# Kernel tuning notes

Hardware: AMD Instinct MI355X
Metric: run time of the kernel (lower is better)

## Reference

```python
import jax, jax.numpy as jnp
import numpy as np

B, T, C, NH = 4, 2048, 1024, 16
D = C // NH  # 64


def setup_inputs() -> dict:
    key = jax.random.key(0)
    ks = jax.random.split(key, 6)
    x = jax.random.normal(ks[0], (B, T, C), dtype=jnp.float32)
    # realistic RoPE tables: interleaved cos/sin over T positions, D head dim
    inv_freq = 1.0 / (10000.0 ** (np.arange(0, D, 2, dtype=np.float32) / D))
    ang = np.arange(T, dtype=np.float32)[:, None] * inv_freq[None, :]  # (T, D/2)
    ang = np.repeat(ang, 2, axis=-1)  # (T, D) interleaved
    pe_cos = jnp.asarray(np.cos(ang))[None, None]  # (1,1,T,D)
    pe_sin = jnp.asarray(np.sin(ang))[None, None]
    pe_scale = jax.random.uniform(ks[1], (1, 1, T, D), dtype=jnp.float32, minval=0.5, maxval=1.5)
    mask = 0.1 * jax.random.normal(ks[2], (1, B, T, T), dtype=jnp.float32)
    w_qkv = jax.random.normal(ks[3], (3 * C, C), dtype=jnp.float32) * (C ** -0.5)
    b_qkv = jax.random.normal(ks[4], (3 * C,), dtype=jnp.float32) * 0.02
    return {"x": x, "pe_cos": pe_cos, "pe_sin": pe_sin, "pe_scale": pe_scale,
            "mask": mask, "w_qkv": w_qkv, "b_qkv": b_qkv}


def _rotate_interleaved(u):
    # even positions <- -odd, odd positions <- even (RoPE interleave)
    u2 = u.reshape(u.shape[:-1] + (-1, 2))
    rot = jnp.stack([-u2[..., 1], u2[..., 0]], axis=-1)
    return rot.reshape(u.shape)


def reference(x, pe_cos, pe_sin, pe_scale, mask, w_qkv, b_qkv):
    b, t, c = x.shape
    qkv = x @ w_qkv.T + b_qkv  # (b, t, 3c)
    q, k, v = jnp.split(qkv, 3, axis=-1)
    # (b, t, nh, d) -> (b, nh, t, d)
    to_heads = lambda u: u.reshape(b, t, NH, D).transpose(0, 2, 1, 3)
    q, k, v = to_heads(q), to_heads(k), to_heads(v)
    # pe tensors (1,1,t,d) broadcast over (b,nh,t,d)
    q = (q * pe_cos + _rotate_interleaved(q) * pe_sin) * pe_scale
    k = (k * pe_cos + _rotate_interleaved(k) * pe_sin) / pe_scale
    scale = 1.0 / ((2.0 * D) ** 0.5)  # original uses scale=1/sqrt(2d)
    scores = jnp.einsum('bhqd,bhkd->bhqk', q, k) * scale
    # torch layout was (nh, b, t, t) + mask (1, b, t, t): mask broadcasts over heads
    scores = scores + jnp.swapaxes(mask, 0, 1)  # mask -> (b, 1, t, t)
    attn = jax.nn.softmax(scores, axis=-1)
    out = jnp.einsum('bhqk,bhkd->bhqd', attn, v)  # (b, nh, t, d)
    return out.transpose(0, 2, 1, 3).reshape(b, t, c)
```

## Files before the change

### kernel.cpp

```cpp
#include <hip/hip_runtime.h>
#include <math.h>

#define NB 4
#define NT 2048
#define NC 1024
#define NHEADS 16
#define HDIM 64

typedef __attribute__((ext_vector_type(8))) _Float16 half8v;
typedef __attribute__((ext_vector_type(2))) __fp16 fp16x2;
typedef __attribute__((ext_vector_type(4))) float f32x4;

#define LOG2E 1.4426950408889634f

__device__ inline unsigned short f2h(float f) {
    _Float16 h = (_Float16)f;
    return __builtin_bit_cast(unsigned short, h);
}
__device__ inline float h2f(unsigned short u) {
    return (float)__builtin_bit_cast(_Float16, u);
}
__device__ inline float exp2fast(float x) {
#if __has_builtin(__builtin_amdgcn_exp2f)
    return __builtin_amdgcn_exp2f(x);
#else
    return exp2f(x);
#endif
}
__device__ inline unsigned int pack2h(float a, float b) {
    fp16x2 p = __builtin_amdgcn_cvt_pkrtz(a, b);
    return __builtin_bit_cast(unsigned int, p);
}

#define AS1C(p) ((const __attribute__((address_space(1))) unsigned int*)(unsigned long long)(const void*)(p))
#define AS3P(p) ((__attribute__((address_space(3))) unsigned int*)(unsigned int)(unsigned long long)(void*)(p))
#define GLL16(gp, lp) __builtin_amdgcn_global_load_lds(AS1C(gp), AS3P(lp), 16, 0, 0)

__global__ __launch_bounds__(256) void conv_f16_kernel(
    const float* __restrict__ in, unsigned short* __restrict__ out, int n4)
{
    const int i = blockIdx.x * 256 + threadIdx.x;
    if (i >= n4) return;
    const float4 f = ((const float4*)in)[i];
    ushort4 h;
    h.x = f2h(f.x); h.y = f2h(f.y); h.z = f2h(f.z); h.w = f2h(f.w);
    ((ushort4*)out)[i] = h;
}

__global__ __launch_bounds__(256) void mask_conv_kernel(
    const float* __restrict__ in, unsigned short* __restrict__ out)
{
    const size_t i = (size_t)blockIdx.x * 256 + threadIdx.x;
    const int row = (int)(i >> 9);
    const int c4 = (int)(i & 511);
    const int ktb = c4 >> 4;
    const int fr = c4 & 15;
    const float* ip = in + (size_t)row * NT + ktb * 64 + fr;
    ushort4 o;
    o.x = f2h(ip[0] * LOG2E);
    o.y = f2h(ip[16] * LOG2E);
    o.z = f2h(ip[32] * LOG2E);
    o.w = f2h(ip[48] * LOG2E);
    ((ushort4*)out)[i] = o;
}

__global__ __launch_bounds__(256) void qkv_gemm_kernel(
    const unsigned short* __restrict__ xf, const unsigned short* __restrict__ wf,
    const float* __restrict__ bias, const float* __restrict__ pe_cos,
    const float* __restrict__ pe_sin, const float* __restrict__ pe_scale,
    unsigned short* __restrict__ qb, unsigned short* __restrict__ kb,
    unsigned short* __restrict__ vtb)
{
    __shared__ __align__(16) unsigned short Ah[128 * 32];
    __shared__ __align__(16) unsigned short Bh[128 * 32];

    const int tid = threadIdx.x;
    const int w = tid >> 6, lane = tid & 63;
    const int g = lane >> 4, fr = lane & 15;
    const int wr = w >> 1, wc = w & 1;

    const int bid = blockIdx.x;
    const int s = (bid & 7) * 192 + (bid >> 3);
    const int m0 = (s & 63) * 128, n0 = (s >> 6) * 128;

    const int c0 = tid, c1 = tid + 256;
    const int r0 = c0 >> 2, r1 = c1 >> 2;
    const int cb0 = ((c0 & 3) * 16) ^ (((r0 >> 1) & 3) << 4);
    const int cb1 = ((c1 & 3) * 16) ^ (((r1 >> 1) & 3) << 4);
    const unsigned short* px0 = xf + (size_t)(m0 + r0) * NC + (cb0 >> 1);
    const unsigned short* px1 = xf + (size_t)(m0 + r1) * NC + (cb1 >> 1);
    const unsigned short* pw0 = wf + (size_t)(n0 + r0) * NC + (cb0 >> 1);
    const unsigned short* pw1 = wf + (size_t)(n0 + r1) * NC + (cb1 >> 1);

    f32x4 acc[4][4];
#pragma unroll
    for (int m = 0; m < 4; ++m)
#pragma unroll
        for (int n = 0; n < 4; ++n) acc[m][n] = (f32x4){0.f, 0.f, 0.f, 0.f};

    for (int k0 = 0; k0 < NC; k0 += 32) {
        __syncthreads();
        GLL16(px0 + k0, (char*)Ah + c0 * 16);
        GLL16(px1 + k0, (char*)Ah + c1 * 16);
        GLL16(pw0 + k0, (char*)Bh + c0 * 16);
        GLL16(pw1 + k0, (char*)Bh + c1 * 16);
        __syncthreads();

        half8v a_f[4], b_f[4];
#pragma unroll
        for (int m = 0; m < 4; ++m) {
            const int r = wr * 64 + m * 16 + fr;
            const int off = r * 64 + ((g * 16) ^ (((r >> 1) & 3) << 4));
            a_f[m] = *(const half8v*)((const char*)Ah + off);
        }
#pragma unroll
        for (int n = 0; n < 4; ++n) {
            const int r = wc * 64 + n * 16 + fr;
            const int off = r * 64 + ((g * 16) ^ (((r >> 1) & 3) << 4));
            b_f[n] = *(const half8v*)((const char*)Bh + off);
        }
#pragma unroll
        for (int m = 0; m < 4; ++m)
#pragma unroll
            for (int n = 0; n < 4; ++n)
                acc[m][n] = __builtin_amdgcn_mfma_f32_16x16x32_f16(a_f[m], b_f[n], acc[m][n], 0, 0, 0);
    }

    const float QSCL = 0.08838834764831845f * LOG2E;
#pragma unroll
    for (int n = 0; n < 4; ++n) {
        const int col = n0 + wc * 64 + n * 16 + fr;
        const int part = col >> 10;
        const int hh = (col & 1023) >> 6;
        const int dd = col & 63;
        const float bv = bias[col];
        if (part < 2) {
            unsigned short* outp = (part == 0) ? qb : kb;
#pragma unroll
            for (int m = 0; m < 4; ++m) {
                const int row0 = m0 + wr * 64 + m * 16 + 4 * g;
                const int bb = row0 >> 11;
                const int t0 = row0 & 2047;
#pragma unroll
                for (int j = 0; j < 4; ++j) {
                    const int t = t0 + j;
                    float val = acc[m][n][j] + bv;
                    const float partner = __shfl_xor(val, 1, 64);
                    const int pidx = t * HDIM + dd;
                    const float cc = pe_cos[pidx], ss = pe_sin[pidx], sc = pe_scale[pidx];
                    const float r = (dd & 1) ? (val * cc + partner * ss)
                                             : (val * cc - partner * ss);
                    val = (part == 0) ? (r * sc * QSCL) : (r / sc);
                    outp[(((size_t)bb * NHEADS + hh) * NT + t) * HDIM + dd] = f2h(val);
                }
            }
        } else {
            const int rowb = m0 + wr * 64;
            const int bb = rowb >> 11;
            const int tb = rowb & 2047;
            unsigned short* vp2 =
                &vtb[(((size_t)bb * NHEADS + hh) * HDIM + dd) * NT + tb];
#pragma unroll
            for (int j = 0; j < 4; ++j) {
                ushort4 sv;
                sv.x = f2h(acc[0][n][j] + bv);
                sv.y = f2h(acc[1][n][j] + bv);
                sv.z = f2h(acc[2][n][j] + bv);
                sv.w = f2h(acc[3][n][j] + bv);
                *(ushort4*)&vp2[(4 * g + j) * 4] = sv;
            }
        }
    }
}

__global__ __launch_bounds__(256) void attn_mfma_kernel(
    const unsigned short* __restrict__ qb, const unsigned short* __restrict__ kb,
    const unsigned short* __restrict__ vtb, const unsigned short* __restrict__ m16,
    float* __restrict__ out)
{
    __shared__ __align__(16) unsigned short Ks[2][64 * 64];
    __shared__ __align__(16) unsigned short Vs[2][64 * 64];
    __shared__ __align__(16) unsigned short Ps[4][16 * 64];

    const int tid = threadIdx.x;
    const int w = tid >> 6, lane = tid & 63;
    const int g = lane >> 4, fr = lane & 15;

    const int bid = blockIdx.x;
    const int s = (bid & 7) * 128 + (bid >> 3);
    const int q0 = (s & 15) * 128;
    const int h = (s >> 4) & 15;
    const int b = s >> 8;

    const size_t bh = (size_t)b * NHEADS + h;
    const unsigned short* qp = qb + (bh * NT + q0 + w * 32) * HDIM;
    const unsigned short* kp = kb + bh * NT * HDIM;
    const unsigned short* vtp = vtb + bh * HDIM * NT;
    const unsigned short* mp = m16 + ((size_t)b * NT + q0 + w * 32) * NT;

    const int sc0 = tid, sc1 = tid + 256;
    const int sr0 = sc0 >> 3, scb0 = ((sc0 & 7) * 16) ^ ((sr0 & 7) << 4);
    const int sr1 = sc1 >> 3, scb1 = ((sc1 & 7) * 16) ^ ((sr1 & 7) << 4);

#define STAGE(buf, kt)                                                          \
    do {                                                                        \
        const unsigned short* ktp_ = kp + (kt) * 64 * HDIM;                     \
        GLL16(ktp_ + sr0 * HDIM + (scb0 >> 1), (char*)Ks[buf] + sc0 * 16);      \
        GLL16(vtp + (size_t)sr0 * NT + (kt) * 64 + (scb0 >> 1),                 \
              (char*)Vs[buf] + sc0 * 16);                                       \
        GLL16(ktp_ + sr1 * HDIM + (scb1 >> 1), (char*)Ks[buf] + sc1 * 16);      \
        GLL16(vtp + (size_t)sr1 * NT + (kt) * 64 + (scb1 >> 1),                 \
              (char*)Vs[buf] + sc1 * 16);                                       \
    } while (0)

    half8v qf[2][2];
#pragma unroll
    for (int m = 0; m < 2; ++m)
#pragma unroll
        for (int kk = 0; kk < 2; ++kk)
            qf[m][kk] = *(const half8v*)(qp + (m * 16 + fr) * HDIM + kk * 32 + g * 8);

    f32x4 acc[2][4];
    float li[2][4], mi[2][4];
#pragma unroll
    for (int m = 0; m < 2; ++m)
#pragma unroll
        for (int j = 0; j < 4; ++j) {
            li[m][j] = 0.f; mi[m][j] = -3.0e38f;
            acc[m][j] = (f32x4){0.f, 0.f, 0.f, 0.f};
        }
    const float THR = 11.541560327111708f;

    STAGE(0, 0);
    __syncthreads();
    int cur = 0;

    for (int kt = 0; kt < NT / 64; ++kt) {
        if (kt + 1 < NT / 64) STAGE(cur ^ 1, kt + 1);

        half8v kf[4][2], vf[4][2];
#pragma unroll
        for (int nt = 0; nt < 4; ++nt) {
            const int r = nt * 16 + fr;
#pragma unroll
            for (int kk = 0; kk < 2; ++kk) {
                const int off = r * 128 + ((kk * 64 + g * 16) ^ ((r & 7) << 4));
                kf[nt][kk] = *(const half8v*)((const char*)Ks[cur] + off);
                vf[nt][kk] = *(const half8v*)((const char*)Vs[cur] + off);
            }
        }

#pragma unroll
        for (int m = 0; m < 2; ++m) {
            f32x4 Sm[4];
#pragma unroll
            for (int nt = 0; nt < 4; ++nt) {
                Sm[nt] = (f32x4){0.f, 0.f, 0.f, 0.f};
#pragma unroll
                for (int kk = 0; kk < 2; ++kk)
                    Sm[nt] = __builtin_amdgcn_mfma_f32_16x16x32_f16(qf[m][kk], kf[nt][kk], Sm[nt], 0, 0, 0);
            }

            float sv[4][4], rmj[4];
#pragma unroll
            for (int j = 0; j < 4; ++j) {
                const ushort4 mv = *(const ushort4*)(
                    mp + (size_t)(m * 16 + 4 * g + j) * NT + kt * 64 + fr * 4);
                sv[j][0] = Sm[0][j] + h2f(mv.x);
                sv[j][1] = Sm[1][j] + h2f(mv.y);
                sv[j][2] = Sm[2][j] + h2f(mv.z);
                sv[j][3] = Sm[3][j] + h2f(mv.w);
                rmj[j] = fmaxf(fmaxf(sv[j][0], sv[j][1]), fmaxf(sv[j][2], sv[j][3]));
            }

            const float worst = fmaxf(fmaxf(rmj[0] - mi[m][0], rmj[1] - mi[m][1]),
                                      fmaxf(rmj[2] - mi[m][2], rmj[3] - mi[m][3]));
            if (!__all(worst <= THR)) {
#pragma unroll
                for (int j = 0; j < 4; ++j) {
                    float rm = rmj[j];
                    rm = fmaxf(rm, __shfl_xor(rm, 1, 64));
                    rm = fmaxf(rm, __shfl_xor(rm, 2, 64));
                    rm = fmaxf(rm, __shfl_xor(rm, 4, 64));
                    rm = fmaxf(rm, __shfl_xor(rm, 8, 64));
                    const float mnew = fmaxf(mi[m][j], rm);
                    const float alpha = exp2fast(mi[m][j] - mnew);
                    li[m][j] *= alpha;
#pragma unroll
                    for (int dt = 0; dt < 4; ++dt) acc[m][dt][j] *= alpha;
                    mi[m][j] = mnew;
                }
            }

#pragma unroll
            for (int j = 0; j < 4; ++j) {
                const int prow = 4 * g + j;
                const float p0 = exp2fast(sv[j][0] - mi[m][j]);
                const float p1 = exp2fast(sv[j][1] - mi[m][j]);
                const float p2 = exp2fast(sv[j][2] - mi[m][j]);
                const float p3 = exp2fast(sv[j][3] - mi[m][j]);
                li[m][j] += (p0 + p1) + (p2 + p3);
                uint2 pw2;
                pw2.x = pack2h(p0, p1);
                pw2.y = pack2h(p2, p3);
                const int off = prow * 128 + ((fr * 8) ^ ((prow & 7) << 4));
                *(uint2*)((char*)Ps[w] + off) = pw2;
            }

            half8v pf[2];
#pragma unroll
            for (int kk = 0; kk < 2; ++kk) {
                const int off = fr * 128 + ((kk * 64 + g * 16) ^ ((fr & 7) << 4));
                pf[kk] = *(const half8v*)((const char*)Ps[w] + off);
            }
#pragma unroll
            for (int dt = 0; dt < 4; ++dt)
#pragma unroll
                for (int kk = 0; kk < 2; ++kk)
                    acc[m][dt] = __builtin_amdgcn_mfma_f32_16x16x32_f16(pf[kk], vf[dt][kk], acc[m][dt], 0, 0, 0);
        }

        __syncthreads();
        cur ^= 1;
    }

#pragma unroll
    for (int m = 0; m < 2; ++m)
#pragma unroll
        for (int j = 0; j < 4; ++j) {
            float lt = li[m][j];
            lt += __shfl_xor(lt, 1, 64);
            lt += __shfl_xor(lt, 2, 64);
            lt += __shfl_xor(lt, 4, 64);
            lt += __shfl_xor(lt, 8, 64);
            const float inv = 1.f / lt;
            const int t = q0 + w * 32 + m * 16 + 4 * g + j;
            float* op = out + (((size_t)b * NT + t) * NHEADS + h) * HDIM;
#pragma unroll
            for (int dt = 0; dt < 4; ++dt) op[dt * 16 + fr] = acc[m][dt][j] * inv;
        }
}

extern "C" void kernel_launch(void* const* d_in, const int* in_sizes, int n_in,
                              void* d_out, int out_size, void* d_ws, size_t ws_size,
                              hipStream_t stream) {
    const float* x        = (const float*)d_in[0];
    const float* pe_cos   = (const float*)d_in[1];
    const float* pe_sin   = (const float*)d_in[2];
    const float* pe_scale = (const float*)d_in[3];
    const float* mask     = (const float*)d_in[4];
    const float* w_qkv    = (const float*)d_in[5];
    const float* b_qkv    = (const float*)d_in[6];
    float* out = (float*)d_out;

    unsigned short* ws = (unsigned short*)d_ws;
    const size_t PER = (size_t)NB * NHEADS * NT * HDIM;
    unsigned short* qbuf = ws;
    unsigned short* kbuf = ws + PER;
    unsigned short* vtbuf = ws + 2 * PER;
    unsigned short* xbuf = ws + 3 * PER;
    unsigned short* wbuf = xbuf + (size_t)NB * NT * NC;
    unsigned short* maskbuf = ws + 3 * PER;

    conv_f16_kernel<<<8192, 256, 0, stream>>>(x, xbuf, (NB * NT * NC) / 4);
    conv_f16_kernel<<<3072, 256, 0, stream>>>(w_qkv, wbuf, (3 * NC * NC) / 4);
    qkv_gemm_kernel<<<1536, 256, 0, stream>>>(xbuf, wbuf, b_qkv,
                                              pe_cos, pe_sin, pe_scale,
                                              qbuf, kbuf, vtbuf);
    mask_conv_kernel<<<16384, 256, 0, stream>>>(mask, maskbuf);
    attn_mfma_kernel<<<1024, 256, 0, stream>>>(qbuf, kbuf, vtbuf, maskbuf, out);
}
```

Measured before the change: 262.5 us.

## Double per-block query tile and share one softmax max per wave tile

Each block now processes 256 query rows (64 per wave) instead of 128, halving the grid to 512 blocks so each staged K/V tile is reused by twice as many queries. The online-softmax running max is also changed from per-row to a single max shared across each 16-row wave tile, computed with a full-wave reduction. This cuts the per-row max reductions and rescaling work. The costs are a doubled accumulator register footprint, which may lower occupancy, and fewer blocks than may be needed to fill all CUs. Using a coarser shared max is still mathematically valid but can reduce numerical headroom when row maxima differ widely.

```diff
diff --git a/kernel.cpp b/kernel.cpp
--- a/kernel.cpp
+++ b/kernel.cpp
@@ -187,16 +187,16 @@
     const int g = lane >> 4, fr = lane & 15;
 
     const int bid = blockIdx.x;
-    const int s = (bid & 7) * 128 + (bid >> 3);
-    const int q0 = (s & 15) * 128;
-    const int h = (s >> 4) & 15;
-    const int b = s >> 8;
+    const int s = (bid & 7) * 64 + (bid >> 3);
+    const int q0 = (s & 7) * 256;
+    const int h = (s >> 3) & 15;
+    const int b = s >> 7;
 
     const size_t bh = (size_t)b * NHEADS + h;
-    const unsigned short* qp = qb + (bh * NT + q0 + w * 32) * HDIM;
+    const unsigned short* qp = qb + (bh * NT + q0 + w * 64) * HDIM;
     const unsigned short* kp = kb + bh * NT * HDIM;
     const unsigned short* vtp = vtb + bh * HDIM * NT;
-    const unsigned short* mp = m16 + ((size_t)b * NT + q0 + w * 32) * NT;
+    const unsigned short* mp = m16 + ((size_t)b * NT + q0 + w * 64) * NT;
 
     const int sc0 = tid, sc1 = tid + 256;
     const int sr0 = sc0 >> 3, scb0 = ((sc0 & 7) * 16) ^ ((sr0 & 7) << 4);
@@ -213,22 +213,24 @@
               (char*)Vs[buf] + sc1 * 16);                                       \
     } while (0)
 
-    half8v qf[2][2];
-#pragma unroll
-    for (int m = 0; m < 2; ++m)
+    half8v qf[4][2];
+#pragma unroll
+    for (int m = 0; m < 4; ++m)
 #pragma unroll
         for (int kk = 0; kk < 2; ++kk)
             qf[m][kk] = *(const half8v*)(qp + (m * 16 + fr) * HDIM + kk * 32 + g * 8);
 
-    f32x4 acc[2][4];
-    float li[2][4], mi[2][4];
-#pragma unroll
-    for (int m = 0; m < 2; ++m)
+    f32x4 acc[4][4];
+    float li[4][4], mi[4];
+#pragma unroll
+    for (int m = 0; m < 4; ++m) {
+        mi[m] = -3.0e38f;
 #pragma unroll
         for (int j = 0; j < 4; ++j) {
-            li[m][j] = 0.f; mi[m][j] = -3.0e38f;
+            li[m][j] = 0.f;
             acc[m][j] = (f32x4){0.f, 0.f, 0.f, 0.f};
         }
+    }
     const float THR = 11.541560327111708f;
 
     STAGE(0, 0);
@@ -251,7 +253,7 @@
         }
 
 #pragma unroll
-        for (int m = 0; m < 2; ++m) {
+        for (int m = 0; m < 4; ++m) {
             f32x4 Sm[4];
 #pragma unroll
             for (int nt = 0; nt < 4; ++nt) {
@@ -261,7 +263,8 @@
                     Sm[nt] = __builtin_amdgcn_mfma_f32_16x16x32_f16(qf[m][kk], kf[nt][kk], Sm[nt], 0, 0, 0);
             }
 
-            float sv[4][4], rmj[4];
+            float sv[4][4];
+            float smax = -3.4e38f;
 #pragma unroll
             for (int j = 0; j < 4; ++j) {
                 const ushort4 mv = *(const ushort4*)(
@@ -270,35 +273,37 @@
                 sv[j][1] = Sm[1][j] + h2f(mv.y);
                 sv[j][2] = Sm[2][j] + h2f(mv.z);
                 sv[j][3] = Sm[3][j] + h2f(mv.w);
-                rmj[j] = fmaxf(fmaxf(sv[j][0], sv[j][1]), fmaxf(sv[j][2], sv[j][3]));
-            }
-
-            const float worst = fmaxf(fmaxf(rmj[0] - mi[m][0], rmj[1] - mi[m][1]),
-                                      fmaxf(rmj[2] - mi[m][2], rmj[3] - mi[m][3]));
-            if (!__all(worst <= THR)) {
+                smax = fmaxf(smax,
+                             fmaxf(fmaxf(sv[j][0], sv[j][1]),
+                                   fmaxf(sv[j][2], sv[j][3])));
+            }
+
+            if (!__all(smax - mi[m] <= THR)) {
+                float rm = smax;
+                rm = fmaxf(rm, __shfl_xor(rm, 1, 64));
+                rm = fmaxf(rm, __shfl_xor(rm, 2, 64));
+                rm = fmaxf(rm, __shfl_xor(rm, 4, 64));
+                rm = fmaxf(rm, __shfl_xor(rm, 8, 64));
+                rm = fmaxf(rm, __shfl_xor(rm, 16, 64));
+                rm = fmaxf(rm, __shfl_xor(rm, 32, 64));
+                const float mnew = fmaxf(mi[m], rm);
+                const float alpha = exp2fast(mi[m] - mnew);
 #pragma unroll
                 for (int j = 0; j < 4; ++j) {
-                    float rm = rmj[j];
-                    rm = fmaxf(rm, __shfl_xor(rm, 1, 64));
-                    rm = fmaxf(rm, __shfl_xor(rm, 2, 64));
-                    rm = fmaxf(rm, __shfl_xor(rm, 4, 64));
-                    rm = fmaxf(rm, __shfl_xor(rm, 8, 64));
-                    const float mnew = fmaxf(mi[m][j], rm);
-                    const float alpha = exp2fast(mi[m][j] - mnew);
                     li[m][j] *= alpha;
 #pragma unroll
                     for (int dt = 0; dt < 4; ++dt) acc[m][dt][j] *= alpha;
-                    mi[m][j] = mnew;
                 }
+                mi[m] = mnew;
             }
 
 #pragma unroll
             for (int j = 0; j < 4; ++j) {
                 const int prow = 4 * g + j;
-                const float p0 = exp2fast(sv[j][0] - mi[m][j]);
-                const float p1 = exp2fast(sv[j][1] - mi[m][j]);
-                const float p2 = exp2fast(sv[j][2] - mi[m][j]);
-                const float p3 = exp2fast(sv[j][3] - mi[m][j]);
+                const float p0 = exp2fast(sv[j][0] - mi[m]);
+                const float p1 = exp2fast(sv[j][1] - mi[m]);
+                const float p2 = exp2fast(sv[j][2] - mi[m]);
+                const float p3 = exp2fast(sv[j][3] - mi[m]);
                 li[m][j] += (p0 + p1) + (p2 + p3);
                 uint2 pw2;
                 pw2.x = pack2h(p0, p1);
@@ -325,7 +330,7 @@
     }
 
 #pragma unroll
-    for (int m = 0; m < 2; ++m)
+    for (int m = 0; m < 4; ++m)
 #pragma unroll
         for (int j = 0; j < 4; ++j) {
             float lt = li[m][j];
@@ -334,7 +339,7 @@
             lt += __shfl_xor(lt, 4, 64);
             lt += __shfl_xor(lt, 8, 64);
             const float inv = 1.f / lt;
-            const int t = q0 + w * 32 + m * 16 + 4 * g + j;
+            const int t = q0 + w * 64 + m * 16 + 4 * g + j;
             float* op = out + (((size_t)b * NT + t) * NHEADS + h) * HDIM;
 #pragma unroll
             for (int dt = 0; dt < 4; ++dt) op[dt * 16 + fr] = acc[m][dt][j] * inv;
@@ -368,5 +373,5 @@
                                               pe_cos, pe_sin, pe_scale,
                                               qbuf, kbuf, vtbuf);
     mask_conv_kernel<<<16384, 256, 0, stream>>>(mask, maskbuf);
-    attn_mfma_kernel<<<1024, 256, 0, stream>>>(qbuf, kbuf, vtbuf, maskbuf, out);
-}
+    attn_mfma_kernel<<<512, 256, 0, stream>>>(qbuf, kbuf, vtbuf, maskbuf, out);
+}
```

Measured after the change: 346.9 us. 1.32x slower.

## Compute transposed scores in attention to keep P in registers, drop LDS round-trip

Applied to the files above, without the earlier changes.

The QK^T MFMA now runs with operands swapped, so each lane holds scores for one query row across several keys. P can then be packed straight into the A-operand of the PV MFMA instead of being written to and read back from LDS. The V^T store order and the mask layout are permuted to match, and the mask conversion uses the generic scaled conversion kernel with a plain row-major layout. Online softmax keeps one max/sum per lane with a wider shuffle reduction, which removes the LDS traffic and per-row bookkeeping but adds a cross-lane shuffle at the end.

```diff
diff --git a/kernel.cpp b/kernel.cpp
--- a/kernel.cpp
+++ b/kernel.cpp
@@ -10,6 +10,7 @@
 typedef __attribute__((ext_vector_type(8))) _Float16 half8v;
 typedef __attribute__((ext_vector_type(2))) __fp16 fp16x2;
 typedef __attribute__((ext_vector_type(4))) float f32x4;
+typedef __attribute__((ext_vector_type(4))) unsigned int u32x4;
 
 #define LOG2E 1.4426950408889634f
 
@@ -37,31 +38,16 @@
 #define GLL16(gp, lp) __builtin_amdgcn_global_load_lds(AS1C(gp), AS3P(lp), 16, 0, 0)
 
 __global__ __launch_bounds__(256) void conv_f16_kernel(
-    const float* __restrict__ in, unsigned short* __restrict__ out, int n4)
+    const float* __restrict__ in, unsigned short* __restrict__ out, int n4,
+    float scale)
 {
     const int i = blockIdx.x * 256 + threadIdx.x;
     if (i >= n4) return;
     const float4 f = ((const float4*)in)[i];
     ushort4 h;
-    h.x = f2h(f.x); h.y = f2h(f.y); h.z = f2h(f.z); h.w = f2h(f.w);
+    h.x = f2h(f.x * scale); h.y = f2h(f.y * scale);
+    h.z = f2h(f.z * scale); h.w = f2h(f.w * scale);
     ((ushort4*)out)[i] = h;
-}
-
-__global__ __launch_bounds__(256) void mask_conv_kernel(
-    const float* __restrict__ in, unsigned short* __restrict__ out)
-{
-    const size_t i = (size_t)blockIdx.x * 256 + threadIdx.x;
-    const int row = (int)(i >> 9);
-    const int c4 = (int)(i & 511);
-    const int ktb = c4 >> 4;
-    const int fr = c4 & 15;
-    const float* ip = in + (size_t)row * NT + ktb * 64 + fr;
-    ushort4 o;
-    o.x = f2h(ip[0] * LOG2E);
-    o.y = f2h(ip[16] * LOG2E);
-    o.z = f2h(ip[32] * LOG2E);
-    o.w = f2h(ip[48] * LOG2E);
-    ((ushort4*)out)[i] = o;
 }
 
 __global__ __launch_bounds__(256) void qkv_gemm_kernel(
@@ -160,15 +146,19 @@
             const int tb = rowb & 2047;
             unsigned short* vp2 =
                 &vtb[(((size_t)bb * NHEADS + hh) * HDIM + dd) * NT + tb];
-#pragma unroll
-            for (int j = 0; j < 4; ++j) {
-                ushort4 sv;
-                sv.x = f2h(acc[0][n][j] + bv);
-                sv.y = f2h(acc[1][n][j] + bv);
-                sv.z = f2h(acc[2][n][j] + bv);
-                sv.w = f2h(acc[3][n][j] + bv);
-                *(ushort4*)&vp2[(4 * g + j) * 4] = sv;
-            }
+            ushort4 s0a, s0b, s1a, s1b;
+            s0a.x = f2h(acc[0][n][0] + bv); s0a.y = f2h(acc[0][n][1] + bv);
+            s0a.z = f2h(acc[0][n][2] + bv); s0a.w = f2h(acc[0][n][3] + bv);
+            s0b.x = f2h(acc[2][n][0] + bv); s0b.y = f2h(acc[2][n][1] + bv);
+            s0b.z = f2h(acc[2][n][2] + bv); s0b.w = f2h(acc[2][n][3] + bv);
+            s1a.x = f2h(acc[1][n][0] + bv); s1a.y = f2h(acc[1][n][1] + bv);
+            s1a.z = f2h(acc[1][n][2] + bv); s1a.w = f2h(acc[1][n][3] + bv);
+            s1b.x = f2h(acc[3][n][0] + bv); s1b.y = f2h(acc[3][n][1] + bv);
+            s1b.z = f2h(acc[3][n][2] + bv); s1b.w = f2h(acc[3][n][3] + bv);
+            *(ushort4*)&vp2[8 * g]          = s0a;
+            *(ushort4*)&vp2[8 * g + 4]      = s0b;
+            *(ushort4*)&vp2[32 + 8 * g]     = s1a;
+            *(ushort4*)&vp2[32 + 8 * g + 4] = s1b;
         }
     }
 }
@@ -180,7 +170,6 @@
 {
     __shared__ __align__(16) unsigned short Ks[2][64 * 64];
     __shared__ __align__(16) unsigned short Vs[2][64 * 64];
-    __shared__ __align__(16) unsigned short Ps[4][16 * 64];
 
     const int tid = threadIdx.x;
     const int w = tid >> 6, lane = tid & 63;
@@ -196,7 +185,7 @@
     const unsigned short* qp = qb + (bh * NT + q0 + w * 32) * HDIM;
     const unsigned short* kp = kb + bh * NT * HDIM;
     const unsigned short* vtp = vtb + bh * HDIM * NT;
-    const unsigned short* mp = m16 + ((size_t)b * NT + q0 + w * 32) * NT;
+    const unsigned short* mp = m16 + ((size_t)b * NT + q0 + w * 32 + fr) * NT;
 
     const int sc0 = tid, sc1 = tid + 256;
     const int sr0 = sc0 >> 3, scb0 = ((sc0 & 7) * 16) ^ ((sr0 & 7) << 4);
@@ -221,14 +210,13 @@
             qf[m][kk] = *(const half8v*)(qp + (m * 16 + fr) * HDIM + kk * 32 + g * 8);
 
     f32x4 acc[2][4];
-    float li[2][4], mi[2][4];
-#pragma unroll
-    for (int m = 0; m < 2; ++m)
-#pragma unroll
-        for (int j = 0; j < 4; ++j) {
-            li[m][j] = 0.f; mi[m][j] = -3.0e38f;
-            acc[m][j] = (f32x4){0.f, 0.f, 0.f, 0.f};
-        }
+    float li[2], mi[2];
+#pragma unroll
+    for (int m = 0; m < 2; ++m) {
+        li[m] = 0.f; mi[m] = -3.0e38f;
+#pragma unroll
+        for (int dt = 0; dt < 4; ++dt) acc[m][dt] = (f32x4){0.f, 0.f, 0.f, 0.f};
+    }
     const float THR = 11.541560327111708f;
 
     STAGE(0, 0);
@@ -258,66 +246,63 @@
                 Sm[nt] = (f32x4){0.f, 0.f, 0.f, 0.f};
 #pragma unroll
                 for (int kk = 0; kk < 2; ++kk)
-                    Sm[nt] = __builtin_amdgcn_mfma_f32_16x16x32_f16(qf[m][kk], kf[nt][kk], Sm[nt], 0, 0, 0);
-            }
-
-            float sv[4][4], rmj[4];
-#pragma unroll
-            for (int j = 0; j < 4; ++j) {
-                const ushort4 mv = *(const ushort4*)(
-                    mp + (size_t)(m * 16 + 4 * g + j) * NT + kt * 64 + fr * 4);
-                sv[j][0] = Sm[0][j] + h2f(mv.x);
-                sv[j][1] = Sm[1][j] + h2f(mv.y);
-                sv[j][2] = Sm[2][j] + h2f(mv.z);
-                sv[j][3] = Sm[3][j] + h2f(mv.w);
-                rmj[j] = fmaxf(fmaxf(sv[j][0], sv[j][1]), fmaxf(sv[j][2], sv[j][3]));
-            }
-
-            const float worst = fmaxf(fmaxf(rmj[0] - mi[m][0], rmj[1] - mi[m][1]),
-                                      fmaxf(rmj[2] - mi[m][2], rmj[3] - mi[m][3]));
-            if (!__all(worst <= THR)) {
+                    Sm[nt] = __builtin_amdgcn_mfma_f32_16x16x32_f16(kf[nt][kk], qf[m][kk], Sm[nt], 0, 0, 0);
+            }
+
+            float sv[4][4];
+            float smax = -3.4e38f;
+            const unsigned short* mq = mp + (size_t)m * 16 * NT + kt * 64;
+#pragma unroll
+            for (int nt = 0; nt < 4; ++nt) {
+                const ushort4 mv = *(const ushort4*)(mq + nt * 16 + 4 * g);
+                sv[nt][0] = Sm[nt][0] + h2f(mv.x);
+                sv[nt][1] = Sm[nt][1] + h2f(mv.y);
+                sv[nt][2] = Sm[nt][2] + h2f(mv.z);
+                sv[nt][3] = Sm[nt][3] + h2f(mv.w);
+                smax = fmaxf(smax,
+                             fmaxf(fmaxf(sv[nt][0], sv[nt][1]),
+                                   fmaxf(sv[nt][2], sv[nt][3])));
+            }
+
+            if (!__all(smax - mi[m] <= THR)) {
+                float rm = smax;
+                rm = fmaxf(rm, __shfl_xor(rm, 1, 64));
+                rm = fmaxf(rm, __shfl_xor(rm, 2, 64));
+                rm = fmaxf(rm, __shfl_xor(rm, 4, 64));
+                rm = fmaxf(rm, __shfl_xor(rm, 8, 64));
+                rm = fmaxf(rm, __shfl_xor(rm, 16, 64));
+                rm = fmaxf(rm, __shfl_xor(rm, 32, 64));
+                const float mnew = fmaxf(mi[m], rm);
+                const float alpha = exp2fast(mi[m] - mnew);
+                li[m] *= alpha;
+#pragma unroll
+                for (int dt = 0; dt < 4; ++dt) acc[m][dt] *= alpha;
+                mi[m] = mnew;
+            }
+
+            float p[4][4];
+            float ps = 0.f;
+#pragma unroll
+            for (int nt = 0; nt < 4; ++nt)
 #pragma unroll
                 for (int j = 0; j < 4; ++j) {
-                    float rm = rmj[j];
-                    rm = fmaxf(rm, __shfl_xor(rm, 1, 64));
-                    rm = fmaxf(rm, __shfl_xor(rm, 2, 64));
-                    rm = fmaxf(rm, __shfl_xor(rm, 4, 64));
-                    rm = fmaxf(rm, __shfl_xor(rm, 8, 64));
-                    const float mnew = fmaxf(mi[m][j], rm);
-                    const float alpha = exp2fast(mi[m][j] - mnew);
-                    li[m][j] *= alpha;
-#pragma unroll
-                    for (int dt = 0; dt < 4; ++dt) acc[m][dt][j] *= alpha;
-                    mi[m][j] = mnew;
+                    p[nt][j] = exp2fast(sv[nt][j] - mi[m]);
+                    ps += p[nt][j];
                 }
-            }
-
-#pragma unroll
-            for (int j = 0; j < 4; ++j) {
-                const int prow = 4 * g + j;
-                const float p0 = exp2fast(sv[j][0] - mi[m][j]);
-                const float p1 = exp2fast(sv[j][1] - mi[m][j]);
-                const float p2 = exp2fast(sv[j][2] - mi[m][j]);
-                const float p3 = exp2fast(sv[j][3] - mi[m][j]);
-                li[m][j] += (p0 + p1) + (p2 + p3);
-                uint2 pw2;
-                pw2.x = pack2h(p0, p1);
-                pw2.y = pack2h(p2, p3);
-                const int off = prow * 128 + ((fr * 8) ^ ((prow & 7) << 4));
-                *(uint2*)((char*)Ps[w] + off) = pw2;
-            }
-
-            half8v pf[2];
-#pragma unroll
-            for (int kk = 0; kk < 2; ++kk) {
-                const int off = fr * 128 + ((kk * 64 + g * 16) ^ ((fr & 7) << 4));
-                pf[kk] = *(const half8v*)((const char*)Ps[w] + off);
-            }
-#pragma unroll
-            for (int dt = 0; dt < 4; ++dt)
-#pragma unroll
-                for (int kk = 0; kk < 2; ++kk)
-                    acc[m][dt] = __builtin_amdgcn_mfma_f32_16x16x32_f16(pf[kk], vf[dt][kk], acc[m][dt], 0, 0, 0);
+            li[m] += ps;
+            u32x4 u0, u1;
+            u0.x = pack2h(p[0][0], p[0][1]); u0.y = pack2h(p[0][2], p[0][3]);
+            u0.z = pack2h(p[2][0], p[2][1]); u0.w = pack2h(p[2][2], p[2][3]);
+            u1.x = pack2h(p[1][0], p[1][1]); u1.y = pack2h(p[1][2], p[1][3]);
+            u1.z = pack2h(p[3][0], p[3][1]); u1.w = pack2h(p[3][2], p[3][3]);
+            const half8v pf0 = __builtin_bit_cast(half8v, u0);
+            const half8v pf1 = __builtin_bit_cast(half8v, u1);
+
+#pragma unroll
+            for (int dt = 0; dt < 4; ++dt) {
+                acc[m][dt] = __builtin_amdgcn_mfma_f32_16x16x32_f16(pf0, vf[dt][0], acc[m][dt], 0, 0, 0);
+                acc[m][dt] = __builtin_amdgcn_mfma_f32_16x16x32_f16(pf1, vf[dt][1], acc[m][dt], 0, 0, 0);
+            }
         }
 
         __syncthreads();
@@ -325,20 +310,20 @@
     }
 
 #pragma unroll
-    for (int m = 0; m < 2; ++m)
+    for (int m = 0; m < 2; ++m) {
+        float lt = li[m];
+        lt += __shfl_xor(lt, 16, 64);
+        lt += __shfl_xor(lt, 32, 64);
 #pragma unroll
         for (int j = 0; j < 4; ++j) {
-            float lt = li[m][j];
-            lt += __shfl_xor(lt, 1, 64);
-            lt += __shfl_xor(lt, 2, 64);
-            lt += __shfl_xor(lt, 4, 64);
-            lt += __shfl_xor(lt, 8, 64);
-            const float inv = 1.f / lt;
+            const float lq = __shfl(lt, 4 * g + j, 64);
+            const float inv = 1.f / lq;
             const int t = q0 + w * 32 + m * 16 + 4 * g + j;
             float* op = out + (((size_t)b * NT + t) * NHEADS + h) * HDIM;
 #pragma unroll
             for (int dt = 0; dt < 4; ++dt) op[dt * 16 + fr] = acc[m][dt][j] * inv;
         }
+    }
 }
 
 extern "C" void kernel_launch(void* const* d_in, const int* in_sizes, int n_in,
@@ -362,11 +347,11 @@
     unsigned short* wbuf = xbuf + (size_t)NB * NT * NC;
     unsigned short* maskbuf = ws + 3 * PER;
 
-    conv_f16_kernel<<<8192, 256, 0, stream>>>(x, xbuf, (NB * NT * NC) / 4);
-    conv_f16_kernel<<<3072, 256, 0, stream>>>(w_qkv, wbuf, (3 * NC * NC) / 4);
+    conv_f16_kernel<<<8192, 256, 0, stream>>>(x, xbuf, (NB * NT * NC) / 4, 1.0f);
+    conv_f16_kernel<<<3072, 256, 0, stream>>>(w_qkv, wbuf, (3 * NC * NC) / 4, 1.0f);
     qkv_gemm_kernel<<<1536, 256, 0, stream>>>(xbuf, wbuf, b_qkv,
                                               pe_cos, pe_sin, pe_scale,
                                               qbuf, kbuf, vtbuf);
-    mask_conv_kernel<<<16384, 256, 0, stream>>>(mask, maskbuf);
+    conv_f16_kernel<<<16384, 256, 0, stream>>>(mask, maskbuf, (NB * NT * NT) / 4, LOG2E);
     attn_mfma_kernel<<<1024, 256, 0, stream>>>(qbuf, kbuf, vtbuf, maskbuf, out);
 }
```

Result: slower. 271.0 us (+3.2%).
